# Optimization experiments

Hardware: AMD Instinct MI355X
Metric: run time of the kernel (lower is better)

The kernel has to match this reference:

```python
import jax, jax.numpy as jnp
import numpy as np

N = 50000
E = 800000
IN_F, HID, OUT_F = 512, 256, 64
KEEP = 0.5  # Dropout(0.5)


def setup_inputs() -> dict:
    key = jax.random.key(0)
    ks = jax.random.split(key, 7)
    X = jax.random.normal(ks[0], (N, IN_F), dtype=jnp.float32)
    # Xavier-uniform-style init for the two layer weights
    lim1 = float(np.sqrt(6.0 / (IN_F + HID)))
    lim2 = float(np.sqrt(6.0 / (HID + OUT_F)))
    W1 = jax.random.uniform(ks[1], (IN_F, HID), jnp.float32, -lim1, lim1)
    W2 = jax.random.uniform(ks[2], (HID, OUT_F), jnp.float32, -lim2, lim2)
    a_row = jnp.sort(jax.random.randint(ks[3], (E,), 0, N)).astype(jnp.int64)
    a_col = jax.random.randint(ks[4], (E,), 0, N).astype(jnp.int64)
    a_val = jax.random.uniform(ks[5], (E,), jnp.float32)
    drop_mask = jax.random.randint(ks[6], (N, HID), 0, 2).astype(jnp.int32)
    return {"X": X, "W1": W1, "W2": W2, "a_row": a_row, "a_col": a_col,
            "a_val": a_val, "drop_mask": drop_mask}


def _spmm(a_row, a_col, a_val, dense):
    # A @ dense where A is [N, N] sparse in COO form: gather + weighted segment-sum
    msgs = a_val[:, None] * dense[a_col]          # [E, d]
    return jax.ops.segment_sum(msgs, a_row, num_segments=N)


def reference(X, W1, W2, a_row, a_col, a_val, drop_mask):
    # layer 1: feature transform + neighbor aggregation
    h = _spmm(a_row, a_col, a_val, X @ W1)        # [N, HID]
    h = jax.nn.relu(h)
    h = h * drop_mask.astype(h.dtype) * (1.0 / KEEP)  # Dropout(0.5), train mode
    # layer 2
    out = _spmm(a_row, a_col, a_val, h @ W2)      # [N, OUT_F]
    return jax.nn.log_softmax(out, axis=1)
```

## Files before the change

### kernel.cpp

```cpp
#include <hip/hip_runtime.h>
#include <hip/hip_bf16.h>
#include <math.h>

#define NN   50000
#define EE   800000
#define INF  512
#define HIDF 256
#define OUTF 64
#define MTILES (NN/16)

using short8 = __attribute__((ext_vector_type(8))) short;
using short4v = __attribute__((ext_vector_type(4))) short;
using f32x4  = __attribute__((ext_vector_type(4))) float;

static __device__ __forceinline__ short f2bf(float f){
  unsigned u = __builtin_bit_cast(unsigned, f);
  u += 0x7fff + ((u >> 16) & 1);
  return (short)(u >> 16);
}
static __device__ __forceinline__ float bf2f(short s){
  unsigned u = ((unsigned)(unsigned short)s) << 16;
  return __builtin_bit_cast(float, u);
}

__global__ void k_prep(const int* __restrict__ a_row, int* __restrict__ row_ptr,
                       const float* __restrict__ W1, short* __restrict__ W1p,
                       const float* __restrict__ W2, short* __restrict__ W2bT){
  int b = blockIdx.x, tid = threadIdx.x;
  if (b < 196){
    int i = b * 256 + tid;
    if (i > NN) return;
    int lo = 0, hi = EE;
    while (lo < hi){ int mid = (lo + hi) >> 1; if (a_row[mid] < i) lo = mid + 1; else hi = mid; }
    row_ptr[i] = lo;
  } else if (b < 708){
    int idx = (b - 196) * 256 + tid;
    int k = idx >> 8, col = idx & 255;
    int kk = k >> 5, k2 = k & 31;
    W1p[((kk << 8) + col) * 32 + k2] = f2bf(W1[idx]);
  } else {
    int idx = (b - 708) * 256 + tid;
    int k = idx >> 6, n = idx & 63;
    W2bT[n * HIDF + k] = f2bf(W2[idx]);
  }
}

__global__ __launch_bounds__(256) void k_gemm1(const float* __restrict__ X,
                                               const short* __restrict__ W1p,
                                               short* __restrict__ XW1b){
  __shared__ short lds[256 * 40];
  int wave = threadIdx.x >> 6, lane = threadIdx.x & 63;
  int l16 = lane & 15, quad = lane >> 4;
  int m0 = blockIdx.x * 128 + wave * 32;
  int r0 = min(m0 + l16, NN - 1);
  int r1 = min(m0 + 16 + l16, NN - 1);
  const float* arow0 = X + (size_t)r0 * INF + quad * 8;
  const float* arow1 = X + (size_t)r1 * INF + quad * 8;

  f32x4 acc0[16], acc1[16];
  #pragma unroll
  for (int t = 0; t < 16; t++){ acc0[t] = (f32x4){0.f,0.f,0.f,0.f}; acc1[t] = (f32x4){0.f,0.f,0.f,0.f}; }

  for (int kk = 0; kk < INF/32; kk++){
    const float4* ap0 = (const float4*)(arow0 + kk * 32);
    const float4* ap1 = (const float4*)(arow1 + kk * 32);
    float4 a00 = ap0[0], a01 = ap0[1];
    float4 a10 = ap1[0], a11 = ap1[1];

    const short* chunk = W1p + kk * (256*32);
    #pragma unroll
    for (int j = 0; j < 4; j++){
      int off16 = j * 256 + threadIdx.x;
      int col = off16 >> 2, kq = threadIdx.x & 3;
      *(short8*)(lds + col * 40 + kq * 8) = *(const short8*)(chunk + off16 * 8);
    }
    __syncthreads();

    short8 af0, af1;
    af0[0]=f2bf(a00.x); af0[1]=f2bf(a00.y); af0[2]=f2bf(a00.z); af0[3]=f2bf(a00.w);
    af0[4]=f2bf(a01.x); af0[5]=f2bf(a01.y); af0[6]=f2bf(a01.z); af0[7]=f2bf(a01.w);
    af1[0]=f2bf(a10.x); af1[1]=f2bf(a10.y); af1[2]=f2bf(a10.z); af1[3]=f2bf(a10.w);
    af1[4]=f2bf(a11.x); af1[5]=f2bf(a11.y); af1[6]=f2bf(a11.z); af1[7]=f2bf(a11.w);
    #pragma unroll
    for (int nt = 0; nt < 16; nt++){
      short8 bf = *(const short8*)(lds + (nt*16 + l16) * 40 + quad * 8);
      acc0[nt] = __builtin_amdgcn_mfma_f32_16x16x32_bf16(af0, bf, acc0[nt], 0, 0, 0);
      acc1[nt] = __builtin_amdgcn_mfma_f32_16x16x32_bf16(af1, bf, acc1[nt], 0, 0, 0);
    }
    __syncthreads();
  }
  #pragma unroll
  for (int nt = 0; nt < 16; nt++){
    int col = nt*16 + l16;
    #pragma unroll
    for (int r = 0; r < 4; r++){
      int row0 = m0 + quad*4 + r;
      int row1 = m0 + 16 + quad*4 + r;
      if (row0 < NN) XW1b[(size_t)row0 * HIDF + col] = f2bf(acc0[nt][r]);
      if (row1 < NN) XW1b[(size_t)row1 * HIDF + col] = f2bf(acc1[nt][r]);
    }
  }
}

__global__ __launch_bounds__(256) void k_spmm1(const int* __restrict__ row_ptr,
                                               const int* __restrict__ a_col,
                                               const float* __restrict__ a_val,
                                               const short* __restrict__ XW1b,
                                               const int* __restrict__ drop_mask,
                                               short* __restrict__ hb){
  int wave = threadIdx.x >> 6, lane = threadIdx.x & 63;
  int r = blockIdx.x * 4 + wave;
  int s = row_ptr[r], e = row_ptr[r+1];
  int g = lane >> 4;
  int c16 = lane & 15;
  float acc[16];
  #pragma unroll
  for (int j = 0; j < 16; j++) acc[j] = 0.f;

  int i = s + g;
  for (; i + 4 < e; i += 8){
    float v0 = a_val[i];     int c0 = a_col[i];
    float v1 = a_val[i+4];   int c1 = a_col[i+4];
    const short* p0 = XW1b + (size_t)c0 * HIDF + c16 * 16;
    const short* p1 = XW1b + (size_t)c1 * HIDF + c16 * 16;
    short8 x0a = *(const short8*)(p0);
    short8 x0b = *(const short8*)(p0 + 8);
    short8 x1a = *(const short8*)(p1);
    short8 x1b = *(const short8*)(p1 + 8);
    #pragma unroll
    for (int j = 0; j < 8; j++){
      acc[j]   += v0 * bf2f(x0a[j]);  acc[j+8] += v0 * bf2f(x0b[j]);
      acc[j]   += v1 * bf2f(x1a[j]);  acc[j+8] += v1 * bf2f(x1b[j]);
    }
  }
  for (; i < e; i += 4){
    float v = a_val[i];  int c = a_col[i];
    const short* p = XW1b + (size_t)c * HIDF + c16 * 16;
    short8 xa = *(const short8*)(p);
    short8 xb = *(const short8*)(p + 8);
    #pragma unroll
    for (int j = 0; j < 8; j++){
      acc[j] += v * bf2f(xa[j]);  acc[j+8] += v * bf2f(xb[j]);
    }
  }
  #pragma unroll
  for (int j = 0; j < 16; j++){
    acc[j] += __shfl_xor(acc[j], 16);
    acc[j] += __shfl_xor(acc[j], 32);
  }
  if (lane < 16){
    const int* dm = drop_mask + (size_t)r * HIDF + c16 * 16;
    short8 o0, o1;
    #pragma unroll
    for (int j = 0; j < 8; j++){
      o0[j] = f2bf(fmaxf(acc[j],   0.f) * (float)dm[j]   * 2.0f);
      o1[j] = f2bf(fmaxf(acc[j+8], 0.f) * (float)dm[j+8] * 2.0f);
    }
    short* hp = hb + (size_t)r * HIDF + c16 * 16;
    *(short8*)(hp)     = o0;
    *(short8*)(hp + 8) = o1;
  }
}

__global__ __launch_bounds__(256) void k_gemm2(const short* __restrict__ A,
                                               const short* __restrict__ BT,
                                               short* __restrict__ C){
  int wave = threadIdx.x >> 6, lane = threadIdx.x & 63;
  int tile_m = blockIdx.x * 4 + wave;
  if (tile_m >= MTILES) return;
  int m0 = tile_m * 16, l16 = lane & 15, quad = lane >> 4;

  f32x4 acc[4];
  #pragma unroll
  for (int t = 0; t < 4; t++) acc[t] = (f32x4){0.f,0.f,0.f,0.f};

  const short* ar = A + (size_t)(m0 + l16) * HIDF + quad * 8;
  for (int kk = 0; kk < HIDF/32; kk++){
    short8 af = *(const short8*)(ar + kk * 32);
    #pragma unroll
    for (int nt = 0; nt < 4; nt++){
      short8 bf = *(const short8*)(BT + (size_t)(nt*16 + l16) * HIDF + kk*32 + quad*8);
      acc[nt] = __builtin_amdgcn_mfma_f32_16x16x32_bf16(af, bf, acc[nt], 0, 0, 0);
    }
  }
  #pragma unroll
  for (int nt = 0; nt < 4; nt++){
    int col = nt*16 + l16;
    #pragma unroll
    for (int r = 0; r < 4; r++)
      C[(size_t)(m0 + quad*4 + r) * OUTF + col] = f2bf(acc[nt][r]);
  }
}

__global__ __launch_bounds__(256) void k_spmm2_lsm(const int* __restrict__ row_ptr,
                                                   const int* __restrict__ a_col,
                                                   const float* __restrict__ a_val,
                                                   const short* __restrict__ HW2b,
                                                   float* __restrict__ out){
  int wave = threadIdx.x >> 6, lane = threadIdx.x & 63;
  int r = blockIdx.x * 4 + wave;
  int s = row_ptr[r], e = row_ptr[r+1];
  int g = lane >> 4;
  int c4 = lane & 15;
  float acc[4] = {0,0,0,0};

  int i = s + g;
  for (; i + 4 < e; i += 8){
    float v0 = a_val[i];    int c0 = a_col[i];
    float v1 = a_val[i+4];  int c1 = a_col[i+4];
    short4v x0 = *(const short4v*)(HW2b + (size_t)c0 * OUTF + c4 * 4);
    short4v x1 = *(const short4v*)(HW2b + (size_t)c1 * OUTF + c4 * 4);
    #pragma unroll
    for (int j = 0; j < 4; j++){ acc[j] += v0 * bf2f(x0[j]); acc[j] += v1 * bf2f(x1[j]); }
  }
  for (; i < e; i += 4){
    float v = a_val[i];  int c = a_col[i];
    short4v x = *(const short4v*)(HW2b + (size_t)c * OUTF + c4 * 4);
    #pragma unroll
    for (int j = 0; j < 4; j++) acc[j] += v * bf2f(x[j]);
  }
  #pragma unroll
  for (int j = 0; j < 4; j++){
    acc[j] += __shfl_xor(acc[j], 16);
    acc[j] += __shfl_xor(acc[j], 32);
  }
  float m = fmaxf(fmaxf(acc[0], acc[1]), fmaxf(acc[2], acc[3]));
  #pragma unroll
  for (int o = 1; o <= 8; o <<= 1) m = fmaxf(m, __shfl_xor(m, o));
  float ssum = expf(acc[0]-m) + expf(acc[1]-m) + expf(acc[2]-m) + expf(acc[3]-m);
  #pragma unroll
  for (int o = 1; o <= 8; o <<= 1) ssum += __shfl_xor(ssum, o);
  float ls = logf(ssum);
  if (lane < 16){
    float4 o4 = { acc[0]-m-ls, acc[1]-m-ls, acc[2]-m-ls, acc[3]-m-ls };
    *(float4*)(out + (size_t)r * OUTF + c4 * 4) = o4;
  }
}

extern "C" void kernel_launch(void* const* d_in, const int* in_sizes, int n_in,
                              void* d_out, int out_size, void* d_ws, size_t ws_size,
                              hipStream_t stream) {
  const float* X      = (const float*)d_in[0];
  const float* W1     = (const float*)d_in[1];
  const float* W2     = (const float*)d_in[2];
  const int*   a_row  = (const int*)d_in[3];
  const int*   a_col  = (const int*)d_in[4];
  const float* a_val  = (const float*)d_in[5];
  const int*   drop   = (const int*)d_in[6];
  float*       out    = (float*)d_out;

  char* ws = (char*)d_ws;
  int*   row_ptr = (int*)  (ws);
  short* W1p     = (short*)(ws + 200704);
  short* W2bT    = (short*)(ws + 462848);
  short* XW1b    = (short*)(ws + 495616);
  short* hb      = (short*)(ws + 26095616);
  short* HW2b    = (short*)(ws + 51695616);

  k_prep<<<772, 256, 0, stream>>>(a_row, row_ptr, W1, W1p, W2, W2bT);
  k_gemm1<<<(NN + 127)/128, 256, 0, stream>>>(X, W1p, XW1b);
  k_spmm1<<<NN/4, 256, 0, stream>>>(row_ptr, a_col, a_val, XW1b, drop, hb);
  k_gemm2<<<(MTILES + 3)/4, 256, 0, stream>>>(hb, W2bT, HW2b);
  k_spmm2_lsm<<<NN/4, 256, 0, stream>>>(row_ptr, a_col, a_val, HW2b, out);
}
```

Measured before the change: 337.4 us.

## Drop LDS staging in gemm1, read W1 fragments directly from global memory

The first GEMM no longer stages W1 chunks through shared memory with block barriers. Each wave now loads its B fragments straight from the prepacked global W1 (which is small and L2-resident) and computes a 16-row tile instead of 32, with a minBlocks launch bound of 3 and twice as many blocks. This removes the LDS writes and syncthreads, and the halved accumulator set lowers register pressure for better occupancy. In exchange, B-fragment reuse across row tiles drops and global/L2 traffic for W1 rises.

```diff
diff --git a/kernel.cpp b/kernel.cpp
--- a/kernel.cpp
+++ b/kernel.cpp
@@ -45,59 +45,40 @@
   }
 }
 
-__global__ __launch_bounds__(256) void k_gemm1(const float* __restrict__ X,
-                                               const short* __restrict__ W1p,
-                                               short* __restrict__ XW1b){
-  __shared__ short lds[256 * 40];
+__global__ __launch_bounds__(256, 3) void k_gemm1(const float* __restrict__ X,
+                                                  const short* __restrict__ W1p,
+                                                  short* __restrict__ XW1b){
   int wave = threadIdx.x >> 6, lane = threadIdx.x & 63;
   int l16 = lane & 15, quad = lane >> 4;
-  int m0 = blockIdx.x * 128 + wave * 32;
-  int r0 = min(m0 + l16, NN - 1);
-  int r1 = min(m0 + 16 + l16, NN - 1);
-  const float* arow0 = X + (size_t)r0 * INF + quad * 8;
-  const float* arow1 = X + (size_t)r1 * INF + quad * 8;
-
-  f32x4 acc0[16], acc1[16];
-  #pragma unroll
-  for (int t = 0; t < 16; t++){ acc0[t] = (f32x4){0.f,0.f,0.f,0.f}; acc1[t] = (f32x4){0.f,0.f,0.f,0.f}; }
+  int m0 = blockIdx.x * 64 + wave * 16;
+  int r = min(m0 + l16, NN - 1);
+  const float* arow = X + (size_t)r * INF + quad * 8;
+  const short* bbase = W1p + l16 * 32 + quad * 8;
+
+  f32x4 acc[16];
+  #pragma unroll
+  for (int t = 0; t < 16; t++) acc[t] = (f32x4){0.f,0.f,0.f,0.f};
 
   for (int kk = 0; kk < INF/32; kk++){
-    const float4* ap0 = (const float4*)(arow0 + kk * 32);
-    const float4* ap1 = (const float4*)(arow1 + kk * 32);
-    float4 a00 = ap0[0], a01 = ap0[1];
-    float4 a10 = ap1[0], a11 = ap1[1];
-
-    const short* chunk = W1p + kk * (256*32);
-    #pragma unroll
-    for (int j = 0; j < 4; j++){
-      int off16 = j * 256 + threadIdx.x;
-      int col = off16 >> 2, kq = threadIdx.x & 3;
-      *(short8*)(lds + col * 40 + kq * 8) = *(const short8*)(chunk + off16 * 8);
-    }
-    __syncthreads();
-
-    short8 af0, af1;
-    af0[0]=f2bf(a00.x); af0[1]=f2bf(a00.y); af0[2]=f2bf(a00.z); af0[3]=f2bf(a00.w);
-    af0[4]=f2bf(a01.x); af0[5]=f2bf(a01.y); af0[6]=f2bf(a01.z); af0[7]=f2bf(a01.w);
-    af1[0]=f2bf(a10.x); af1[1]=f2bf(a10.y); af1[2]=f2bf(a10.z); af1[3]=f2bf(a10.w);
-    af1[4]=f2bf(a11.x); af1[5]=f2bf(a11.y); af1[6]=f2bf(a11.z); af1[7]=f2bf(a11.w);
+    const float4* ap = (const float4*)(arow + kk * 32);
+    float4 a0 = ap[0], a1 = ap[1];
+    short8 af;
+    af[0]=f2bf(a0.x); af[1]=f2bf(a0.y); af[2]=f2bf(a0.z); af[3]=f2bf(a0.w);
+    af[4]=f2bf(a1.x); af[5]=f2bf(a1.y); af[6]=f2bf(a1.z); af[7]=f2bf(a1.w);
+    const short* bk = bbase + kk * (256*32);
     #pragma unroll
     for (int nt = 0; nt < 16; nt++){
-      short8 bf = *(const short8*)(lds + (nt*16 + l16) * 40 + quad * 8);
-      acc0[nt] = __builtin_amdgcn_mfma_f32_16x16x32_bf16(af0, bf, acc0[nt], 0, 0, 0);
-      acc1[nt] = __builtin_amdgcn_mfma_f32_16x16x32_bf16(af1, bf, acc1[nt], 0, 0, 0);
-    }
-    __syncthreads();
+      short8 bf = *(const short8*)(bk + nt * (16*32));
+      acc[nt] = __builtin_amdgcn_mfma_f32_16x16x32_bf16(af, bf, acc[nt], 0, 0, 0);
+    }
   }
   #pragma unroll
   for (int nt = 0; nt < 16; nt++){
     int col = nt*16 + l16;
     #pragma unroll
-    for (int r = 0; r < 4; r++){
-      int row0 = m0 + quad*4 + r;
-      int row1 = m0 + 16 + quad*4 + r;
-      if (row0 < NN) XW1b[(size_t)row0 * HIDF + col] = f2bf(acc0[nt][r]);
-      if (row1 < NN) XW1b[(size_t)row1 * HIDF + col] = f2bf(acc1[nt][r]);
+    for (int rr = 0; rr < 4; rr++){
+      int row = m0 + quad*4 + rr;
+      if (row < NN) XW1b[(size_t)row * HIDF + col] = f2bf(acc[nt][rr]);
     }
   }
 }
@@ -258,7 +239,7 @@
   short* HW2b    = (short*)(ws + 51695616);
 
   k_prep<<<772, 256, 0, stream>>>(a_row, row_ptr, W1, W1p, W2, W2bT);
-  k_gemm1<<<(NN + 127)/128, 256, 0, stream>>>(X, W1p, XW1b);
+  k_gemm1<<<(NN + 63)/64, 256, 0, stream>>>(X, W1p, XW1b);
   k_spmm1<<<NN/4, 256, 0, stream>>>(row_ptr, a_col, a_val, XW1b, drop, hb);
   k_gemm2<<<(MTILES + 3)/4, 256, 0, stream>>>(hb, W2bT, HW2b);
   k_spmm2_lsm<<<NN/4, 256, 0, stream>>>(row_ptr, a_col, a_val, HW2b, out);
```

Result: slower. 347.5 us (+3.0%).
